# Optimization experiments

Hardware: AMD Instinct MI355X
Metric: run time of the kernel (lower is better)

Reference implementation:

```python
import jax, jax.numpy as jnp
import numpy as np

PI = np.pi
TAU = 1.0        # self.tau
TAU_V = 10.0     # self.tau_v
TAU_CONN = 10.0  # self.tau_conn
TAU_E = 1000.0   # self.tau_e
GW = PI / 4      # gauss_width
GH = 3.0         # gauss_height
LR = 10000.0     # hebbian lr
SPIKE_NUM = 4    # keep_top_n count
NORM_FAC_HD = 1.0


def period_bound(d):
    # wrap to (-pi, pi]
    return (d + PI) % (2.0 * PI) - PI


def dist(d):
    d = period_bound(d)
    return jnp.where(d > PI, d - 2.0 * PI, d)


def setup_inputs() -> dict:
    key = jax.random.key(0)
    ks = jax.random.split(key, 8)
    P, num, L = 20000, 256, 30
    return {
        "conn_bearing": jnp.abs(jax.random.normal(ks[0], (P, num, L), jnp.float32) * 0.1),
        "r": jax.random.uniform(ks[1], (num,), jnp.float32) * 0.1,
        "u": jax.random.uniform(ks[2], (num,), jnp.float32) * 0.5,
        "v": jax.random.uniform(ks[3], (num,), jnp.float32) * 0.1,
        "r_hpc": jax.random.uniform(ks[4], (P,), jnp.float32),
        "r_bearing": jax.random.uniform(ks[5], (L,), jnp.float32),
        "pos_estimate": jnp.zeros((1,), jnp.float32),
        "angular_velocity": jnp.float32(0.3),
        "HD": jnp.float32(0.5),
        "sen2HD_stre": jnp.float32(1.0),
        "shared_t": jnp.arange(2, dtype=jnp.float32) * 0.1,  # [0, dt]
        "noise_hd": jax.random.normal(ks[6], (num,), jnp.float32) * 0.01,
        "noise_bearing": jax.random.normal(ks[7], (L,), jnp.float32) * 0.01,
        "dt": 0.1,
    }


def reference(conn_bearing, r, u, v, r_hpc, r_bearing, pos_estimate,
              angular_velocity, HD, sen2HD_stre, shared_t,
              noise_hd, noise_bearing, dt):
    # One HdOVCModel.update step with get_HD=0, noise_stre=0.0, train=2.
    P, num, L = conn_bearing.shape
    k = 0.8 / num * 20.0
    J0 = 1.0 / num * 20.0
    m = 0.84 * TAU / TAU_V
    x = jnp.linspace(-PI, PI, num + 1)[:-1]  # ring preferred directions

    # ring connectivity kernel + its FFT (precomputed in __init__)
    d0 = dist(jnp.abs(x[0] - x))
    conn = J0 * jnp.exp(-0.5 * jnp.square(d0 / GW)) / (2.0 * PI * GW ** 2)
    conn_fft = jnp.fft.fft(conn)

    # get_center(r, x) == angle(sum(exp(1j x) * r)), done in reals
    center = jnp.arctan2(jnp.sum(jnp.sin(x) * r), jnp.sum(jnp.cos(x) * r))

    # self_motion_integrate (noise_stre = 0)
    pos_e = pos_estimate + (period_bound(center - pos_estimate) / TAU_E + angular_velocity) * dt
    pos_est = period_bound(pos_e)  # [1]
    motion_input = GH * jnp.exp(-0.25 * jnp.square(dist(x - pos_est) / GW))  # [num]
    Iext = motion_input  # get_HD == 0 branch (input_HD(HD) unused)

    # bearing input via hippocampal place weighting
    r_place = r_hpc[:P]
    index = jnp.argmax(r_place)
    norm_r = jnp.where(r_place == 0, 0.0, r_place / jnp.sum(r_place))
    # fused matmul [P,num,L]@[L] then weighted sum over P
    input_bearing = jnp.einsum('pnl,l,p->n', conn_bearing, r_bearing, norm_r)

    # recurrent ring input via circular convolution (FFT)
    Irec = jnp.real(jnp.fft.ifft(jnp.fft.fft(r) * conn_fft))
    input_total = Iext + Irec + input_bearing * sen2HD_stre

    # derivative() is linear with CONSTANT coupling terms (uses self.u/self.v,
    # not the integrated state), so odeint has an exact closed form:
    # du/dt = (-u + Cu)/tau, dv/dt = (-v + Cv)/tau_v
    t = shared_t[1] - shared_t[0]
    Cu = input_total - v
    Cv = m * u
    u_sol = Cu + (u - Cu) * jnp.exp(-t / TAU)
    v_sol = Cv + (v - Cv) * jnp.exp(-t / TAU_V)
    u_new = jnp.maximum(u_sol, 0.0)
    v_new = v_sol
    r1 = jnp.square(u_new)
    r_new = r1 / (1.0 + k * jnp.sum(r1))

    # conn_update (train == 2): gather row -> top-k Hebb -> normalize -> scatter
    cb_row = conn_bearing[index]                         # [num, L]
    r_hd = r_new * (1.0 + jnp.abs(noise_hd))
    topv = jax.lax.top_k(r_hd, SPIKE_NUM)[0]
    r_learn = jnp.where(r_hd >= topv[-1], r_hd, 0.0)     # keep_top_n
    rb = r_bearing + jnp.abs(noise_bearing)
    corr = jnp.outer(r_learn, rb)                        # [num, L]
    d_b = LR * corr * cb_row / TAU_CONN * dt
    cb = cb_row + d_b
    cb = NORM_FAC_HD * cb / jnp.sum(cb, axis=1, keepdims=True)  # normalize_rows
    conn_bearing_new = conn_bearing.at[index].set(cb)

    return r_new, u_new, v_new, conn_bearing_new
```

## Files before the change

kernel.cpp:

```cpp
#include <hip/hip_runtime.h>

#define PI_F 3.14159265358979323846f
#define TWO_PI_F 6.28318530717958647692f

#define TAU_F 1.0f
#define TAU_V_F 10.0f
#define TAU_CONN_F 10.0f
#define TAU_E_F 1000.0f
#define GW_F (PI_F / 4.0f)
#define GH_F 3.0f
#define LR_F 10000.0f

#define NUMN 256
#define LB 30
#define SLAB (NUMN * LB)
#define SLAB4 (SLAB / 4)

__device__ __forceinline__ float pbf(float d) {
  float m = fmodf(d + PI_F, TWO_PI_F);
  if (m < 0.f) m += TWO_PI_F;
  return m - PI_F;
}

__global__ __launch_bounds__(256) void k_reduce_hpc(const float* __restrict__ r_hpc,
                                                    int P, float* __restrict__ ws) {
  __shared__ float ssum[256];
  __shared__ float smax[256];
  __shared__ int simax[256];
  int t = threadIdx.x;
  float s = 0.f;
  float bm = -1e30f;
  int bi = 0x7fffffff;
  for (int i = t; i < P; i += 256) {
    float v = r_hpc[i];
    s += v;
    if (v > bm) { bm = v; bi = i; }
  }
  ssum[t] = s; smax[t] = bm; simax[t] = bi;
  __syncthreads();
  for (int off = 128; off > 0; off >>= 1) {
    if (t < off) {
      ssum[t] += ssum[t + off];
      float vo = smax[t + off]; int io = simax[t + off];
      if (vo > smax[t] || (vo == smax[t] && io < simax[t])) { smax[t] = vo; simax[t] = io; }
    }
    __syncthreads();
  }
  if (t == 0) {
    ws[0] = ssum[0];
    ((int*)ws)[1] = simax[0];
  }
}

__global__ __launch_bounds__(256) void k_main(const float* __restrict__ cb,
                                              const float* __restrict__ r_hpc,
                                              const float* __restrict__ r_bearing,
                                              const float* __restrict__ ws_scal,
                                              float* __restrict__ partial,
                                              float* __restrict__ out_cb,
                                              int P, int chunk) {
  __shared__ __align__(16) float slab[SLAB];
  __shared__ float rbs[32];
  int t = threadIdx.x;
  int blk = blockIdx.x;
  if (t < LB) rbs[t] = r_bearing[t];
  float S = ws_scal[0];
  float acc = 0.f;
  int p0 = blk * chunk;
  int p1 = p0 + chunk; if (p1 > P) p1 = P;
  for (int p = p0; p < p1; ++p) {
    const float4* in4 = (const float4*)(cb + (size_t)p * SLAB);
    float4* o4 = (float4*)(out_cb + (size_t)p * SLAB);
    float4* s4 = (float4*)slab;
    for (int i = t; i < SLAB4; i += 256) {
      float4 v = in4[i];
      s4[i] = v;
      o4[i] = v;
    }
    __syncthreads();
    float rp = r_hpc[p];
    float w = (rp == 0.f) ? 0.f : rp / S;
    const float* row = slab + t * LB;
    float dot = 0.f;
#pragma unroll
    for (int l = 0; l < LB; ++l) dot += row[l] * rbs[l];
    acc += w * dot;
    __syncthreads();
  }
  partial[(size_t)blk * NUMN + t] = acc;
}

__global__ __launch_bounds__(256) void k_reduce_partial(const float* __restrict__ partial,
                                                        float* __restrict__ p2, int nb) {
  int t = threadIdx.x;
  int j = blockIdx.x;
  float s = 0.f;
  for (int b = j; b < nb; b += 64) s += partial[(size_t)b * NUMN + t];
  p2[(size_t)j * NUMN + t] = s;
}

__device__ __forceinline__ float block_reduce_sum(float val, float* red, int t) {
  red[t] = val;
  __syncthreads();
  for (int off = 128; off > 0; off >>= 1) {
    if (t < off) red[t] += red[t + off];
    __syncthreads();
  }
  float r0 = red[0];
  __syncthreads();
  return r0;
}

__global__ __launch_bounds__(256) void k_finish(
    const float* __restrict__ cb,
    const float* __restrict__ r, const float* __restrict__ u, const float* __restrict__ v,
    const float* __restrict__ noise_hd,
    const float* __restrict__ r_bearing, const float* __restrict__ noise_bearing,
    const float* __restrict__ pos_estimate, const float* __restrict__ angular_velocity,
    const float* __restrict__ sen2HD_stre, const float* __restrict__ shared_t,
    const float* __restrict__ dtp,
    const float* __restrict__ ws_scal, const float* __restrict__ p2,
    float* __restrict__ out) {
  __shared__ float red[256];
  __shared__ float rL[256], connL[256], rhdL[256];
  __shared__ float rbL[32];
  __shared__ float bc[8];
  int t = threadIdx.x;
  int index = ((const int*)ws_scal)[1];

  float ib = 0.f;
  for (int j = 0; j < 64; ++j) ib += p2[(size_t)j * NUMN + t];

  float x = -PI_F + (float)t * (TWO_PI_F / 256.f);
  float rt = r[t];
  rL[t] = rt;

  float ssin = block_reduce_sum(sinf(x) * rt, red, t);
  float scos = block_reduce_sum(cosf(x) * rt, red, t);

  if (t == 0) {
    float center = atan2f(ssin, scos);
    float pe = pos_estimate[0];
    float dtv = dtp[0];
    float pos_e = pe + (pbf(center - pe) / TAU_E_F + angular_velocity[0]) * dtv;
    bc[0] = pbf(pos_e);
  }
  __syncthreads();
  float pos_est = bc[0];

  {
    float J0 = 20.f / 256.f;
    float dmin = fminf((float)t, 256.f - (float)t) * (TWO_PI_F / 256.f);
    float q = dmin / GW_F;
    connL[t] = J0 * expf(-0.5f * q * q) / (TWO_PI_F * GW_F * GW_F);
  }
  __syncthreads();

  float Irec = 0.f;
  for (int m2 = 0; m2 < 256; ++m2) Irec += rL[m2] * connL[(t - m2) & 255];

  float dd = pbf(x - pos_est);
  float qq = dd / GW_F;
  float Iext = GH_F * expf(-0.25f * qq * qq);

  float input_total = Iext + Irec + ib * sen2HD_stre[0];
  float tstep = shared_t[1] - shared_t[0];
  float e1 = expf(-tstep / TAU_F);
  float e2 = expf(-tstep / TAU_V_F);
  float mcoef = 0.84f * TAU_F / TAU_V_F;

  float ut = u[t], vt = v[t];
  float Cu = input_total - vt;
  float Cv = mcoef * ut;
  float u_sol = Cu + (ut - Cu) * e1;
  float v_sol = Cv + (vt - Cv) * e2;
  float u_new = fmaxf(u_sol, 0.f);
  float r1 = u_new * u_new;
  float s1 = block_reduce_sum(r1, red, t);
  float kcoef = 0.8f / 256.f * 20.f;
  float r_new = r1 / (1.f + kcoef * s1);

  out[t] = r_new;
  out[256 + t] = u_new;
  out[512 + t] = v_sol;

  rhdL[t] = r_new * (1.f + fabsf(noise_hd[t]));
  if (t < LB) rbL[t] = r_bearing[t] + fabsf(noise_bearing[t]);
  __syncthreads();

  if (t == 0) {
    int e0 = -1, e1i = -1, e2i = -1, e3 = -1;
    float thr = 0.f;
    for (int pass = 0; pass < 4; ++pass) {
      float bm = -1e30f; int bi = -1;
      for (int i2 = 0; i2 < 256; ++i2) {
        if (i2 == e0 || i2 == e1i || i2 == e2i || i2 == e3) continue;
        float vv = rhdL[i2];
        if (vv > bm) { bm = vv; bi = i2; }
      }
      if (pass == 0) e0 = bi; else if (pass == 1) e1i = bi; else if (pass == 2) e2i = bi; else e3 = bi;
      thr = bm;
    }
    bc[1] = thr;
  }
  __syncthreads();
  float thr = bc[1];
  float r_learn = (rhdL[t] >= thr) ? rhdL[t] : 0.f;

  float dtv = dtp[0];
  float fac = (LR_F / TAU_CONN_F) * dtv;
  const float* rowp = cb + ((size_t)index * NUMN + t) * LB;
  float vals[LB];
  float s = 0.f;
#pragma unroll
  for (int l = 0; l < LB; ++l) {
    float vv = rowp[l] * (1.f + fac * r_learn * rbL[l]);
    vals[l] = vv;
    s += vv;
  }
  float inv = 1.f / s;
  float* orow = out + 768 + ((size_t)index * NUMN + t) * LB;
#pragma unroll
  for (int l = 0; l < LB; ++l) orow[l] = vals[l] * inv;
}

extern "C" void kernel_launch(void* const* d_in, const int* in_sizes, int n_in,
                              void* d_out, int out_size, void* d_ws, size_t ws_size,
                              hipStream_t stream) {
  const float* conn_bearing = (const float*)d_in[0];
  const float* r            = (const float*)d_in[1];
  const float* u            = (const float*)d_in[2];
  const float* v            = (const float*)d_in[3];
  const float* r_hpc        = (const float*)d_in[4];
  const float* r_bearing    = (const float*)d_in[5];
  const float* pos_estimate = (const float*)d_in[6];
  const float* angular_vel  = (const float*)d_in[7];
  const float* sen2HD       = (const float*)d_in[9];
  const float* shared_t     = (const float*)d_in[10];
  const float* noise_hd     = (const float*)d_in[11];
  const float* noise_bear   = (const float*)d_in[12];
  const float* dtp          = (const float*)d_in[13];

  int P = in_sizes[4];

  float* out = (float*)d_out;
  float* ws = (float*)d_ws;

  const int OFF_P2 = 16;
  const int OFF_PART = OFF_P2 + 64 * NUMN;

  int nb = 2000;
  {
    size_t avail = ws_size / 4;
    if (avail < (size_t)OFF_PART + NUMN) {
      nb = 1;
    } else {
      size_t maxnb = (avail - OFF_PART) / NUMN;
      if ((size_t)nb > maxnb) nb = (int)maxnb;
      if (nb < 1) nb = 1;
    }
  }
  int chunk = (P + nb - 1) / nb;

  k_reduce_hpc<<<1, 256, 0, stream>>>(r_hpc, P, ws);
  k_main<<<nb, 256, 0, stream>>>(conn_bearing, r_hpc, r_bearing, ws,
                                 ws + OFF_PART, out + 768, P, chunk);
  k_reduce_partial<<<64, 256, 0, stream>>>(ws + OFF_PART, ws + OFF_P2, nb);
  k_finish<<<1, 256, 0, stream>>>(conn_bearing, r, u, v, noise_hd, r_bearing, noise_bear,
                                  pos_estimate, angular_vel, sen2HD, shared_t, dtp,
                                  ws, ws + OFF_P2, out);
}
```

Baseline: 368.0 us.

## Replace slab-staged main loop with grid-stride float4 streaming and deferred bearing dot

The main kernel no longer stages each 256x30 slab in shared memory with two barriers per P. Each thread now owns a fixed float4 position within the slab (grid size chosen as a multiple of 15 so the position stays constant under the grid stride). It accumulates r_hpc-weighted sums of the four floats and applies the r_bearing dot product once at the end through shared-memory atomics. This removes LDS traffic and synchronisation from the streaming copy, giving a pure coalesced copy plus FMAs, at the cost of a per-iteration scalar r_hpc load and a constraint on grid size.

```diff
diff --git a/kernel.cpp b/kernel.cpp
--- a/kernel.cpp
+++ b/kernel.cpp
@@ -16,6 +16,8 @@
 #define SLAB (NUMN * LB)
 #define SLAB4 (SLAB / 4)
 
+typedef float fx4 __attribute__((ext_vector_type(4)));
+
 __device__ __forceinline__ float pbf(float d) {
   float m = fmodf(d + PI_F, TWO_PI_F);
   if (m < 0.f) m += TWO_PI_F;
@@ -52,42 +54,52 @@
   }
 }
 
-__global__ __launch_bounds__(256) void k_main(const float* __restrict__ cb,
-                                              const float* __restrict__ r_hpc,
-                                              const float* __restrict__ r_bearing,
-                                              const float* __restrict__ ws_scal,
-                                              float* __restrict__ partial,
-                                              float* __restrict__ out_cb,
-                                              int P, int chunk) {
-  __shared__ __align__(16) float slab[SLAB];
-  __shared__ float rbs[32];
-  int t = threadIdx.x;
-  int blk = blockIdx.x;
-  if (t < LB) rbs[t] = r_bearing[t];
+__global__ __launch_bounds__(256, 4) void k_main(const float* __restrict__ cb,
+                                                 const float* __restrict__ r_hpc,
+                                                 const float* __restrict__ r_bearing,
+                                                 const float* __restrict__ ws_scal,
+                                                 float* __restrict__ partial,
+                                                 float* __restrict__ out_cb,
+                                                 int P) {
+  int t = threadIdx.x;
+  size_t tid4 = (size_t)blockIdx.x * 256 + t;
+  size_t T = (size_t)gridDim.x * 256;
+  int q4 = (int)(tid4 % 1920);
+  int p = (int)(tid4 / 1920);
+  int PSTEP = (int)(T / 1920);
   float S = ws_scal[0];
-  float acc = 0.f;
-  int p0 = blk * chunk;
-  int p1 = p0 + chunk; if (p1 > P) p1 = P;
-  for (int p = p0; p < p1; ++p) {
-    const float4* in4 = (const float4*)(cb + (size_t)p * SLAB);
-    float4* o4 = (float4*)(out_cb + (size_t)p * SLAB);
-    float4* s4 = (float4*)slab;
-    for (int i = t; i < SLAB4; i += 256) {
-      float4 v = in4[i];
-      s4[i] = v;
-      o4[i] = v;
-    }
-    __syncthreads();
+
+  const fx4* __restrict__ in4 = (const fx4*)cb;
+  fx4* __restrict__ o4 = (fx4*)out_cb;
+  size_t TOT4 = (size_t)P * SLAB4;
+
+  float a0 = 0.f, a1 = 0.f, a2 = 0.f, a3 = 0.f;
+
+#pragma unroll 4
+  for (size_t i = tid4; i < TOT4; i += T, p += PSTEP) {
+    fx4 v = in4[i];
+    o4[i] = v;
     float rp = r_hpc[p];
-    float w = (rp == 0.f) ? 0.f : rp / S;
-    const float* row = slab + t * LB;
-    float dot = 0.f;
-#pragma unroll
-    for (int l = 0; l < LB; ++l) dot += row[l] * rbs[l];
-    acc += w * dot;
-    __syncthreads();
-  }
-  partial[(size_t)blk * NUMN + t] = acc;
+    float wg = (rp == 0.f) ? 0.f : rp / S;
+    a0 += wg * v.x;
+    a1 += wg * v.y;
+    a2 += wg * v.z;
+    a3 += wg * v.w;
+  }
+
+  __shared__ float buf[NUMN];
+  buf[t] = 0.f;
+  __syncthreads();
+  int f0 = 4 * q4;
+  {
+    int f, n;
+    f = f0 + 0; n = f / 30; atomicAdd(&buf[n], a0 * r_bearing[f - 30 * n]);
+    f = f0 + 1; n = f / 30; atomicAdd(&buf[n], a1 * r_bearing[f - 30 * n]);
+    f = f0 + 2; n = f / 30; atomicAdd(&buf[n], a2 * r_bearing[f - 30 * n]);
+    f = f0 + 3; n = f / 30; atomicAdd(&buf[n], a3 * r_bearing[f - 30 * n]);
+  }
+  __syncthreads();
+  partial[(size_t)blockIdx.x * NUMN + t] = buf[t];
 }
 
 __global__ __launch_bounds__(256) void k_reduce_partial(const float* __restrict__ partial,
@@ -249,22 +261,22 @@
   const int OFF_P2 = 16;
   const int OFF_PART = OFF_P2 + 64 * NUMN;
 
-  int nb = 2000;
+  int nb = 1920;
   {
     size_t avail = ws_size / 4;
-    if (avail < (size_t)OFF_PART + NUMN) {
-      nb = 1;
+    if (avail < (size_t)OFF_PART + 15 * NUMN) {
+      nb = 15;
     } else {
       size_t maxnb = (avail - OFF_PART) / NUMN;
       if ((size_t)nb > maxnb) nb = (int)maxnb;
-      if (nb < 1) nb = 1;
+      nb -= nb % 15;
+      if (nb < 15) nb = 15;
     }
   }
-  int chunk = (P + nb - 1) / nb;
 
   k_reduce_hpc<<<1, 256, 0, stream>>>(r_hpc, P, ws);
   k_main<<<nb, 256, 0, stream>>>(conn_bearing, r_hpc, r_bearing, ws,
-                                 ws + OFF_PART, out + 768, P, chunk);
+                                 ws + OFF_PART, out + 768, P);
   k_reduce_partial<<<64, 256, 0, stream>>>(ws + OFF_PART, ws + OFF_P2, nb);
   k_finish<<<1, 256, 0, stream>>>(conn_bearing, r, u, v, noise_hd, r_bearing, noise_bear,
                                   pos_estimate, angular_vel, sen2HD, shared_t, dtp,
```

Result: faster. 357.6 us (-2.8%).
